# Kernel tuning notes

Measured on AMD Instinct MI355X. Metric: run time of the kernel, lower is better.

Reference implementation:

```python
import jax, jax.numpy as jnp
import numpy as np

B, T, C, HS = 4, 4096, 1024, 64


def setup_inputs() -> dict:
    key = jax.random.key(0)
    kx, kq, kk, kv = jax.random.split(key, 4)
    x = jax.random.normal(kx, (B, T, C), dtype=jnp.float32)
    s = 1.0 / np.sqrt(C)
    Wq = jax.random.normal(kq, (C, HS), dtype=jnp.float32) * s
    Wk = jax.random.normal(kk, (C, HS), dtype=jnp.float32) * s
    Wv = jax.random.normal(kv, (C, HS), dtype=jnp.float32) * s
    return {"x": x, "Wq": Wq, "Wk": Wk, "Wv": Wv}


def reference(x, Wq, Wk, Wv):
    # q,k,v: [B, T, HS]
    q = x @ Wq
    k = x @ Wk
    v = x @ Wv
    scale = k.shape[-1] ** -0.5
    # full T x T causal attention scores, as the torch module materializes
    scores = jnp.einsum('bqh,bkh->bqk', q, k) * scale  # [B, T, T]
    t = x.shape[1]
    causal = jnp.tril(jnp.ones((t, t), dtype=bool))
    scores = jnp.where(causal[None, :, :], scores, -jnp.inf)
    wei = jax.nn.softmax(scores, axis=-1)  # dropout = 0.0 (eval)
    out = jnp.einsum('bqk,bkh->bqh', wei, v)  # [B, T, HS]
    return out
```

## Files before the change

kernel.cpp:

```cpp
#include <hip/hip_runtime.h>
#include <math.h>

#define BB 4
#define TT 4096
#define CC 1024
#define HS 64
#define MM (BB*TT)

typedef __attribute__((ext_vector_type(8))) short short8;
typedef __attribute__((ext_vector_type(4))) float f32x4;
typedef __attribute__((ext_vector_type(4))) unsigned short ushort4v;

__device__ __forceinline__ unsigned short f2bf(float f) {
    union { float f; unsigned u; } v; v.f = f;
    return (unsigned short)((v.u + 0x7fffu + ((v.u >> 16) & 1u)) >> 16);
}

__global__ __launch_bounds__(256) void prep_kernel(
    const float* __restrict__ Wq, const float* __restrict__ Wk,
    const float* __restrict__ Wv, unsigned short* __restrict__ Wt)
{
    const int which = blockIdx.x >> 4;
    const int k0 = (blockIdx.x & 15) * 64;
    const float* __restrict__ W = (which == 0) ? Wq : (which == 1) ? Wk : Wv;
    const float scale = (which == 0) ? 0.125f : 1.0f;
    __shared__ unsigned short lds[64][65];
    const int t = threadIdx.x;
    #pragma unroll
    for (int i = 0; i < 16; i++) {
        int idx = t + 256 * i;
        int r = idx >> 6, n = idx & 63;
        lds[r][n] = f2bf(W[(size_t)(k0 + r) * 64 + n] * scale);
    }
    __syncthreads();
    #pragma unroll
    for (int i = 0; i < 16; i++) {
        int idx = t + 256 * i;
        int n = idx >> 6, r = idx & 63;
        Wt[(which << 16) + (n << 10) + k0 + r] = lds[r][n];
    }
}

__global__ __launch_bounds__(256, 2) void qkv_mfma(
    const float* __restrict__ x, const unsigned short* __restrict__ Wt,
    unsigned short* __restrict__ qb, unsigned short* __restrict__ kb,
    unsigned short* __restrict__ vT)
{
    const int rt = blockIdx.x;
    __shared__ unsigned short xs[32][136];
    __shared__ unsigned short ws[192][136];

    const int t = threadIdx.x;
    const int w = t >> 6;
    const int lane = t & 63;
    const int quad = lane >> 4;
    const int c = lane & 15;

    float4 xreg[4];
    short8 wreg[12];
    #pragma unroll
    for (int i = 0; i < 4; i++) {
        int idx = t + 256 * i;
        int r = idx >> 5, c4 = (idx & 31) * 4;
        xreg[i] = *(const float4*)(x + (size_t)(rt * 32 + r) * CC + c4);
    }
    #pragma unroll
    for (int i = 0; i < 12; i++) {
        int idx = t + 256 * i;
        int n = idx >> 4, c8 = (idx & 15) * 8;
        wreg[i] = *(const short8*)(Wt + (size_t)n * CC + c8);
    }

    f32x4 acc[2][3];
    #pragma unroll
    for (int mt = 0; mt < 2; mt++)
        #pragma unroll
        for (int j = 0; j < 3; j++) acc[mt][j] = (f32x4){0.f, 0.f, 0.f, 0.f};

    for (int k0 = 0; k0 < CC; k0 += 128) {
        __syncthreads();
        #pragma unroll
        for (int i = 0; i < 4; i++) {
            int idx = t + 256 * i;
            int r = idx >> 5, c4 = (idx & 31) * 4;
            ushort4v p = { f2bf(xreg[i].x), f2bf(xreg[i].y), f2bf(xreg[i].z), f2bf(xreg[i].w) };
            *(ushort4v*)&xs[r][c4] = p;
        }
        #pragma unroll
        for (int i = 0; i < 12; i++) {
            int idx = t + 256 * i;
            int n = idx >> 4, c8 = (idx & 15) * 8;
            *(short8*)&ws[n][c8] = wreg[i];
        }
        if (k0 + 128 < CC) {
            #pragma unroll
            for (int i = 0; i < 4; i++) {
                int idx = t + 256 * i;
                int r = idx >> 5, c4 = (idx & 31) * 4;
                xreg[i] = *(const float4*)(x + (size_t)(rt * 32 + r) * CC + k0 + 128 + c4);
            }
            #pragma unroll
            for (int i = 0; i < 12; i++) {
                int idx = t + 256 * i;
                int n = idx >> 4, c8 = (idx & 15) * 8;
                wreg[i] = *(const short8*)(Wt + (size_t)n * CC + k0 + 128 + c8);
            }
        }
        __syncthreads();
        #pragma unroll
        for (int ks = 0; ks < 4; ks++) {
            short8 af[2], bf[3];
            #pragma unroll
            for (int mt = 0; mt < 2; mt++)
                af[mt] = *(const short8*)&xs[16 * mt + c][ks * 32 + quad * 8];
            #pragma unroll
            for (int j = 0; j < 3; j++)
                bf[j] = *(const short8*)&ws[16 * (w + 4 * j) + c][ks * 32 + quad * 8];
            #pragma unroll
            for (int mt = 0; mt < 2; mt++)
                #pragma unroll
                for (int j = 0; j < 3; j++)
                    acc[mt][j] = __builtin_amdgcn_mfma_f32_16x16x32_bf16(af[mt], bf[j], acc[mt][j], 0, 0, 0);
        }
    }

    __syncthreads();
    unsigned short (*vtb)[72] = (unsigned short (*)[72])ws;
    #pragma unroll
    for (int mt = 0; mt < 2; mt++) {
        int grow = rt * 32 + 16 * mt + quad * 4;
        #pragma unroll
        for (int reg = 0; reg < 4; reg++) {
            qb[(size_t)(grow + reg) * HS + 16 * w + c] = f2bf(acc[mt][0][reg]);
            kb[(size_t)(grow + reg) * HS + 16 * w + c] = f2bf(acc[mt][1][reg]);
            vtb[16 * w + c][16 * mt + quad * 4 + reg] = f2bf(acc[mt][2][reg]);
        }
    }
    __syncthreads();
    {
        const int b  = rt >> 7;
        const int t0 = (rt & 127) * 32;
        int d = t >> 2, c8 = (t & 3) * 8;
        short8 v0 = *(const short8*)&vtb[d][c8];
        *(short8*)(vT + (size_t)b * HS * TT + (size_t)d * TT + t0 + c8) = v0;
    }
}

__global__ __launch_bounds__(256, 4) void attn_mfma(
    const unsigned short* __restrict__ qb, const unsigned short* __restrict__ kb,
    const unsigned short* __restrict__ vT, float* __restrict__ Opart,
    float* __restrict__ lpart)
{
    const int bid = blockIdx.x;
    const int qt = (TT / 64 - 1) - (bid >> 4);
    const int j  = (bid >> 2) & 3;
    const int b  = bid & 3;

    __shared__ unsigned short ks[64][72];
    __shared__ unsigned short vt[64][72];
    __shared__ unsigned short ps[4][16][72];

    const int t = threadIdx.x;
    const int w = t >> 6;
    const int lane = t & 63;
    const int quad = lane >> 4;
    const int c = lane & 15;
    const int qrow = qt * 64 + 16 * w;

    short8 aq[2];
    #pragma unroll
    for (int kstep = 0; kstep < 2; kstep++)
        aq[kstep] = *(const short8*)(qb + (size_t)(b * TT + qrow + c) * HS + kstep * 32 + quad * 8);

    const int nkt = (qt >= j) ? ((qt - j) >> 2) + 1 : 0;
    const unsigned short* Kb = kb + (size_t)b * TT * HS;
    const unsigned short* Vb = vT + (size_t)b * HS * TT;

    const int srow = t >> 3;
    const int sc8  = (t & 7) * 8;

    short8 kreg[2], vreg[2];
    if (nkt > 0) {
        const int kt0 = j * 64;
        #pragma unroll
        for (int i = 0; i < 2; i++) {
            kreg[i] = *(const short8*)(Kb + (size_t)(kt0 + srow + 32 * i) * HS + sc8);
            vreg[i] = *(const short8*)(Vb + (size_t)(srow + 32 * i) * TT + kt0 + sc8);
        }
    }

    float l[4] = {0.f, 0.f, 0.f, 0.f};
    f32x4 oacc[4];
    #pragma unroll
    for (int dt = 0; dt < 4; dt++) oacc[dt] = (f32x4){0.f, 0.f, 0.f, 0.f};

    for (int i = 0; i < nkt; i++) {
        const int kt = j + 4 * i;
        const int kt0 = kt * 64;
        __syncthreads();
        #pragma unroll
        for (int ii = 0; ii < 2; ii++) {
            *(short8*)&ks[srow + 32 * ii][sc8] = kreg[ii];
            *(short8*)&vt[srow + 32 * ii][sc8] = vreg[ii];
        }
        if (i + 1 < nkt) {
            const int nb = kt0 + 256;
            #pragma unroll
            for (int ii = 0; ii < 2; ii++) {
                kreg[ii] = *(const short8*)(Kb + (size_t)(nb + srow + 32 * ii) * HS + sc8);
                vreg[ii] = *(const short8*)(Vb + (size_t)(srow + 32 * ii) * TT + nb + sc8);
            }
        }
        __syncthreads();

        f32x4 sc[4];
        #pragma unroll
        for (int st = 0; st < 4; st++) sc[st] = (f32x4){0.f, 0.f, 0.f, 0.f};
        #pragma unroll
        for (int kstep = 0; kstep < 2; kstep++) {
            #pragma unroll
            for (int st = 0; st < 4; st++) {
                short8 bf = *(const short8*)&ks[16 * st + c][kstep * 32 + quad * 8];
                sc[st] = __builtin_amdgcn_mfma_f32_16x16x32_bf16(aq[kstep], bf, sc[st], 0, 0, 0);
            }
        }
        if (kt == qt) {
            #pragma unroll
            for (int st = 0; st < 4; st++)
                #pragma unroll
                for (int reg = 0; reg < 4; reg++) {
                    int kg = kt0 + 16 * st + c;
                    int qg = qrow + quad * 4 + reg;
                    float p = (kg <= qg) ? __expf(sc[st][reg]) : 0.f;
                    sc[st][reg] = p;
                    l[reg] += p;
                }
        } else {
            #pragma unroll
            for (int st = 0; st < 4; st++)
                #pragma unroll
                for (int reg = 0; reg < 4; reg++) {
                    float p = __expf(sc[st][reg]);
                    sc[st][reg] = p;
                    l[reg] += p;
                }
        }
        #pragma unroll
        for (int st = 0; st < 4; st++)
            #pragma unroll
            for (int reg = 0; reg < 4; reg++)
                ps[w][quad * 4 + reg][16 * st + c] = f2bf(sc[st][reg]);

        #pragma unroll
        for (int kstep = 0; kstep < 2; kstep++) {
            short8 ap = *(const short8*)&ps[w][c][kstep * 32 + quad * 8];
            #pragma unroll
            for (int dt = 0; dt < 4; dt++) {
                short8 bv = *(const short8*)&vt[16 * dt + c][kstep * 32 + quad * 8];
                oacc[dt] = __builtin_amdgcn_mfma_f32_16x16x32_bf16(ap, bv, oacc[dt], 0, 0, 0);
            }
        }
    }

    #pragma unroll
    for (int reg = 0; reg < 4; reg++)
        #pragma unroll
        for (int msk = 1; msk < 16; msk <<= 1)
            l[reg] += __shfl_xor(l[reg], msk);

    float* __restrict__ Oj = Opart + (size_t)j * MM * HS;
    #pragma unroll
    for (int dt = 0; dt < 4; dt++)
        #pragma unroll
        for (int reg = 0; reg < 4; reg++)
            Oj[(size_t)(b * TT + qrow + quad * 4 + reg) * HS + 16 * dt + c] = oacc[dt][reg];
    if (c == 0)
        #pragma unroll
        for (int reg = 0; reg < 4; reg++)
            lpart[(size_t)j * MM + b * TT + qrow + quad * 4 + reg] = l[reg];
}

__global__ __launch_bounds__(256) void combine_kernel(
    const float* __restrict__ Opart, const float* __restrict__ lpart,
    float* __restrict__ out)
{
    const int id = blockIdx.x * 256 + threadIdx.x;
    const int row = id >> 4;
    float l = lpart[row] + lpart[MM + row] + lpart[2 * MM + row] + lpart[3 * MM + row];
    const float4* O = (const float4*)Opart;
    const size_t stride = (size_t)MM * HS / 4;
    float4 a = O[id], b = O[id + stride], c = O[id + 2 * stride], d = O[id + 3 * stride];
    float inv = 1.f / l;
    float4 r;
    r.x = (a.x + b.x + c.x + d.x) * inv;
    r.y = (a.y + b.y + c.y + d.y) * inv;
    r.z = (a.z + b.z + c.z + d.z) * inv;
    r.w = (a.w + b.w + c.w + d.w) * inv;
    ((float4*)out)[id] = r;
}

extern "C" void kernel_launch(void* const* d_in, const int* in_sizes, int n_in,
                              void* d_out, int out_size, void* d_ws, size_t ws_size,
                              hipStream_t stream) {
    const float* x  = (const float*)d_in[0];
    const float* Wq = (const float*)d_in[1];
    const float* Wk = (const float*)d_in[2];
    const float* Wv = (const float*)d_in[3];
    float* out = (float*)d_out;

    unsigned short* Wt   = (unsigned short*)d_ws;
    unsigned short* qbuf = Wt + 3 * 64 * 1024;
    unsigned short* kbuf = qbuf + (size_t)MM * HS;
    unsigned short* vTb  = kbuf + (size_t)MM * HS;
    float* Opart = (float*)(vTb + (size_t)MM * HS);
    float* lpart = Opart + 4 * (size_t)MM * HS;

    prep_kernel<<<48, 256, 0, stream>>>(Wq, Wk, Wv, Wt);
    qkv_mfma<<<MM / 32, 256, 0, stream>>>(x, Wt, qbuf, kbuf, vTb);
    attn_mfma<<<BB * (TT / 64) * 4, 256, 0, stream>>>(qbuf, kbuf, vTb, Opart, lpart);
    combine_kernel<<<1024, 256, 0, stream>>>(Opart, lpart, out);
}
```

Before: 136.6 us.

## Retile QKV and attention kernels with register weights, transposed MFMA, larger query tiles

The QKV projection now keeps weight fragments in registers straight from global memory and works on 64-row tiles with double-buffered x in LDS. Attention handles 128 query rows per block with two 16-row subtiles per wave. It computes S^T so the probability fragments can be fed into the PV MFMA from registers, dropping the LDS round trip for P, and permutes V in LDS to match that layout. Opart is stored transposed (d-major), and the combine kernel transposes it back through LDS. These changes trade more register pressure and fewer blocks for less LDS traffic and more data reuse per block.

```diff
diff --git a/kernel.cpp b/kernel.cpp
--- a/kernel.cpp
+++ b/kernel.cpp
@@ -8,6 +8,7 @@
 #define MM (BB*TT)
 
 typedef __attribute__((ext_vector_type(8))) short short8;
+typedef __attribute__((ext_vector_type(4))) short short4v;
 typedef __attribute__((ext_vector_type(4))) float f32x4;
 typedef __attribute__((ext_vector_type(4))) unsigned short ushort4v;
 
@@ -41,14 +42,13 @@
     }
 }
 
-__global__ __launch_bounds__(256, 2) void qkv_mfma(
+__global__ __launch_bounds__(256) void qkv_mfma(
     const float* __restrict__ x, const unsigned short* __restrict__ Wt,
     unsigned short* __restrict__ qb, unsigned short* __restrict__ kb,
     unsigned short* __restrict__ vT)
 {
     const int rt = blockIdx.x;
-    __shared__ unsigned short xs[32][136];
-    __shared__ unsigned short ws[192][136];
+    __shared__ unsigned short xs[2][64][72];
 
     const int t = threadIdx.x;
     const int w = t >> 6;
@@ -56,247 +56,311 @@
     const int quad = lane >> 4;
     const int c = lane & 15;
 
+    const unsigned short* wb[3];
+    #pragma unroll
+    for (int jj = 0; jj < 3; jj++)
+        wb[jj] = Wt + (size_t)((w + 4 * jj) * 16 + c) * CC + quad * 8;
+
     float4 xreg[4];
-    short8 wreg[12];
     #pragma unroll
     for (int i = 0; i < 4; i++) {
         int idx = t + 256 * i;
-        int r = idx >> 5, c4 = (idx & 31) * 4;
-        xreg[i] = *(const float4*)(x + (size_t)(rt * 32 + r) * CC + c4);
-    }
-    #pragma unroll
-    for (int i = 0; i < 12; i++) {
-        int idx = t + 256 * i;
-        int n = idx >> 4, c8 = (idx & 15) * 8;
-        wreg[i] = *(const short8*)(Wt + (size_t)n * CC + c8);
-    }
-
-    f32x4 acc[2][3];
-    #pragma unroll
-    for (int mt = 0; mt < 2; mt++)
-        #pragma unroll
-        for (int j = 0; j < 3; j++) acc[mt][j] = (f32x4){0.f, 0.f, 0.f, 0.f};
-
-    for (int k0 = 0; k0 < CC; k0 += 128) {
-        __syncthreads();
+        xreg[i] = *(const float4*)(x + (size_t)(rt * 64 + (idx >> 4)) * CC + (idx & 15) * 4);
+    }
+    short8 wf[3][2];
+    #pragma unroll
+    for (int jj = 0; jj < 3; jj++)
+        #pragma unroll
+        for (int ks2 = 0; ks2 < 2; ks2++)
+            wf[jj][ks2] = *(const short8*)(wb[jj] + ks2 * 32);
+
+    f32x4 acc[4][3];
+    #pragma unroll
+    for (int mt = 0; mt < 4; mt++)
+        #pragma unroll
+        for (int jj = 0; jj < 3; jj++) acc[mt][jj] = (f32x4){0.f, 0.f, 0.f, 0.f};
+
+    for (int k0 = 0; k0 < CC; k0 += 64) {
+        const int p = (k0 >> 6) & 1;
         #pragma unroll
         for (int i = 0; i < 4; i++) {
             int idx = t + 256 * i;
-            int r = idx >> 5, c4 = (idx & 31) * 4;
-            ushort4v p = { f2bf(xreg[i].x), f2bf(xreg[i].y), f2bf(xreg[i].z), f2bf(xreg[i].w) };
-            *(ushort4v*)&xs[r][c4] = p;
-        }
-        #pragma unroll
-        for (int i = 0; i < 12; i++) {
-            int idx = t + 256 * i;
-            int n = idx >> 4, c8 = (idx & 15) * 8;
-            *(short8*)&ws[n][c8] = wreg[i];
-        }
-        if (k0 + 128 < CC) {
+            int r = idx >> 4, c4 = (idx & 15) * 4;
+            ushort4v pk = { f2bf(xreg[i].x), f2bf(xreg[i].y), f2bf(xreg[i].z), f2bf(xreg[i].w) };
+            *(ushort4v*)&xs[p][r][c4] = pk;
+        }
+        if (k0 + 64 < CC) {
             #pragma unroll
             for (int i = 0; i < 4; i++) {
                 int idx = t + 256 * i;
-                int r = idx >> 5, c4 = (idx & 31) * 4;
-                xreg[i] = *(const float4*)(x + (size_t)(rt * 32 + r) * CC + k0 + 128 + c4);
-            }
-            #pragma unroll
-            for (int i = 0; i < 12; i++) {
-                int idx = t + 256 * i;
-                int n = idx >> 4, c8 = (idx & 15) * 8;
-                wreg[i] = *(const short8*)(Wt + (size_t)n * CC + k0 + 128 + c8);
+                xreg[i] = *(const float4*)(x + (size_t)(rt * 64 + (idx >> 4)) * CC + k0 + 64 + (idx & 15) * 4);
             }
         }
         __syncthreads();
-        #pragma unroll
-        for (int ks = 0; ks < 4; ks++) {
-            short8 af[2], bf[3];
-            #pragma unroll
-            for (int mt = 0; mt < 2; mt++)
-                af[mt] = *(const short8*)&xs[16 * mt + c][ks * 32 + quad * 8];
-            #pragma unroll
-            for (int j = 0; j < 3; j++)
-                bf[j] = *(const short8*)&ws[16 * (w + 4 * j) + c][ks * 32 + quad * 8];
-            #pragma unroll
-            for (int mt = 0; mt < 2; mt++)
-                #pragma unroll
-                for (int j = 0; j < 3; j++)
-                    acc[mt][j] = __builtin_amdgcn_mfma_f32_16x16x32_bf16(af[mt], bf[j], acc[mt][j], 0, 0, 0);
+        short8 wn[3][2];
+        if (k0 + 64 < CC) {
+            #pragma unroll
+            for (int jj = 0; jj < 3; jj++)
+                #pragma unroll
+                for (int ks2 = 0; ks2 < 2; ks2++)
+                    wn[jj][ks2] = *(const short8*)(wb[jj] + k0 + 64 + ks2 * 32);
+        }
+        #pragma unroll
+        for (int ks2 = 0; ks2 < 2; ks2++) {
+            short8 af[4];
+            #pragma unroll
+            for (int mt = 0; mt < 4; mt++)
+                af[mt] = *(const short8*)&xs[p][16 * mt + c][ks2 * 32 + quad * 8];
+            #pragma unroll
+            for (int mt = 0; mt < 4; mt++)
+                #pragma unroll
+                for (int jj = 0; jj < 3; jj++)
+                    acc[mt][jj] = __builtin_amdgcn_mfma_f32_16x16x32_bf16(af[mt], wf[jj][ks2], acc[mt][jj], 0, 0, 0);
+        }
+        if (k0 + 64 < CC) {
+            #pragma unroll
+            for (int jj = 0; jj < 3; jj++)
+                #pragma unroll
+                for (int ks2 = 0; ks2 < 2; ks2++)
+                    wf[jj][ks2] = wn[jj][ks2];
         }
     }
 
     __syncthreads();
-    unsigned short (*vtb)[72] = (unsigned short (*)[72])ws;
-    #pragma unroll
-    for (int mt = 0; mt < 2; mt++) {
-        int grow = rt * 32 + 16 * mt + quad * 4;
+    unsigned short (*vtb)[72] = xs[0];
+    #pragma unroll
+    for (int mt = 0; mt < 4; mt++) {
         #pragma unroll
         for (int reg = 0; reg < 4; reg++) {
-            qb[(size_t)(grow + reg) * HS + 16 * w + c] = f2bf(acc[mt][0][reg]);
-            kb[(size_t)(grow + reg) * HS + 16 * w + c] = f2bf(acc[mt][1][reg]);
-            vtb[16 * w + c][16 * mt + quad * 4 + reg] = f2bf(acc[mt][2][reg]);
+            int lrow = 16 * mt + quad * 4 + reg;
+            size_t grow = (size_t)(rt * 64 + lrow);
+            qb[grow * HS + 16 * w + c] = f2bf(acc[mt][0][reg]);
+            kb[grow * HS + 16 * w + c] = f2bf(acc[mt][1][reg]);
+            vtb[16 * w + c][lrow] = f2bf(acc[mt][2][reg]);
         }
     }
     __syncthreads();
     {
-        const int b  = rt >> 7;
-        const int t0 = (rt & 127) * 32;
-        int d = t >> 2, c8 = (t & 3) * 8;
-        short8 v0 = *(const short8*)&vtb[d][c8];
-        *(short8*)(vT + (size_t)b * HS * TT + (size_t)d * TT + t0 + c8) = v0;
-    }
-}
-
-__global__ __launch_bounds__(256, 4) void attn_mfma(
+        const int b  = rt >> 6;
+        const int t0 = (rt & 63) * 64;
+        #pragma unroll
+        for (int i = 0; i < 2; i++) {
+            int idx = t + 256 * i;
+            int d = idx >> 3, c8 = (idx & 7) * 8;
+            *(short8*)(vT + ((size_t)b * HS + d) * TT + t0 + c8) = *(const short8*)&vtb[d][c8];
+        }
+    }
+}
+
+__global__ __launch_bounds__(256, 2) void attn_mfma(
     const unsigned short* __restrict__ qb, const unsigned short* __restrict__ kb,
     const unsigned short* __restrict__ vT, float* __restrict__ Opart,
     float* __restrict__ lpart)
 {
     const int bid = blockIdx.x;
-    const int qt = (TT / 64 - 1) - (bid >> 4);
+    const int qt = (TT / 128 - 1) - (bid >> 4);
     const int j  = (bid >> 2) & 3;
     const int b  = bid & 3;
 
     __shared__ unsigned short ks[64][72];
     __shared__ unsigned short vt[64][72];
-    __shared__ unsigned short ps[4][16][72];
 
     const int t = threadIdx.x;
     const int w = t >> 6;
     const int lane = t & 63;
     const int quad = lane >> 4;
     const int c = lane & 15;
-    const int qrow = qt * 64 + 16 * w;
-
-    short8 aq[2];
-    #pragma unroll
-    for (int kstep = 0; kstep < 2; kstep++)
-        aq[kstep] = *(const short8*)(qb + (size_t)(b * TT + qrow + c) * HS + kstep * 32 + quad * 8);
-
-    const int nkt = (qt >= j) ? ((qt - j) >> 2) + 1 : 0;
+    const int qrow = qt * 128 + 32 * w;
+
+    short8 aq[2][2];
+    #pragma unroll
+    for (int qt2 = 0; qt2 < 2; qt2++)
+        #pragma unroll
+        for (int ksd = 0; ksd < 2; ksd++)
+            aq[qt2][ksd] = *(const short8*)(qb + (size_t)(b * TT + qrow + 16 * qt2 + c) * HS + ksd * 32 + quad * 8);
+
+    const int lastkt = 2 * qt + 1;
+    const int nkt = (lastkt >= j) ? ((lastkt - j) >> 2) + 1 : 0;
     const unsigned short* Kb = kb + (size_t)b * TT * HS;
     const unsigned short* Vb = vT + (size_t)b * HS * TT;
-
-    const int srow = t >> 3;
-    const int sc8  = (t & 7) * 8;
 
     short8 kreg[2], vreg[2];
     if (nkt > 0) {
         const int kt0 = j * 64;
         #pragma unroll
         for (int i = 0; i < 2; i++) {
-            kreg[i] = *(const short8*)(Kb + (size_t)(kt0 + srow + 32 * i) * HS + sc8);
-            vreg[i] = *(const short8*)(Vb + (size_t)(srow + 32 * i) * TT + kt0 + sc8);
-        }
-    }
-
-    float l[4] = {0.f, 0.f, 0.f, 0.f};
-    f32x4 oacc[4];
-    #pragma unroll
-    for (int dt = 0; dt < 4; dt++) oacc[dt] = (f32x4){0.f, 0.f, 0.f, 0.f};
-
-    for (int i = 0; i < nkt; i++) {
-        const int kt = j + 4 * i;
-        const int kt0 = kt * 64;
+            int idx = t + 256 * i;
+            int row = idx >> 3, c8 = (idx & 7) * 8;
+            kreg[i] = *(const short8*)(Kb + (size_t)(kt0 + row) * HS + c8);
+            vreg[i] = *(const short8*)(Vb + (size_t)row * TT + kt0 + c8);
+        }
+    }
+
+    float lsum[2] = {0.f, 0.f};
+    f32x4 oacc[2][4];
+    #pragma unroll
+    for (int qt2 = 0; qt2 < 2; qt2++)
+        #pragma unroll
+        for (int dt = 0; dt < 4; dt++) oacc[qt2][dt] = (f32x4){0.f, 0.f, 0.f, 0.f};
+
+    for (int it = 0; it < nkt; it++) {
+        const int kt0 = (j + 4 * it) * 64;
         __syncthreads();
         #pragma unroll
-        for (int ii = 0; ii < 2; ii++) {
-            *(short8*)&ks[srow + 32 * ii][sc8] = kreg[ii];
-            *(short8*)&vt[srow + 32 * ii][sc8] = vreg[ii];
-        }
-        if (i + 1 < nkt) {
+        for (int i = 0; i < 2; i++) {
+            int idx = t + 256 * i;
+            int row = idx >> 3, c8 = (idx & 7) * 8;
+            *(short8*)&ks[row][c8] = kreg[i];
+            int t32 = c8 & 32, r32 = c8 & 31;
+            int p0 = t32 + ((r32 & 8) << 1) + ((r32 >> 4) << 2);
+            short8 v = vreg[i];
+            short4v lo = { v[0], v[1], v[2], v[3] };
+            short4v hi = { v[4], v[5], v[6], v[7] };
+            *(short4v*)&vt[row][p0]     = lo;
+            *(short4v*)&vt[row][p0 + 8] = hi;
+        }
+        if (it + 1 < nkt) {
             const int nb = kt0 + 256;
             #pragma unroll
-            for (int ii = 0; ii < 2; ii++) {
-                kreg[ii] = *(const short8*)(Kb + (size_t)(nb + srow + 32 * ii) * HS + sc8);
-                vreg[ii] = *(const short8*)(Vb + (size_t)(srow + 32 * ii) * TT + nb + sc8);
+            for (int i = 0; i < 2; i++) {
+                int idx = t + 256 * i;
+                int row = idx >> 3, c8 = (idx & 7) * 8;
+                kreg[i] = *(const short8*)(Kb + (size_t)(nb + row) * HS + c8);
+                vreg[i] = *(const short8*)(Vb + (size_t)row * TT + nb + c8);
             }
         }
         __syncthreads();
 
-        f32x4 sc[4];
-        #pragma unroll
-        for (int st = 0; st < 4; st++) sc[st] = (f32x4){0.f, 0.f, 0.f, 0.f};
-        #pragma unroll
-        for (int kstep = 0; kstep < 2; kstep++) {
-            #pragma unroll
-            for (int st = 0; st < 4; st++) {
-                short8 bf = *(const short8*)&ks[16 * st + c][kstep * 32 + quad * 8];
-                sc[st] = __builtin_amdgcn_mfma_f32_16x16x32_bf16(aq[kstep], bf, sc[st], 0, 0, 0);
-            }
-        }
-        if (kt == qt) {
+        if (kt0 <= qrow + 31) {
+            f32x4 sc[4][2];
             #pragma unroll
             for (int st = 0; st < 4; st++)
                 #pragma unroll
-                for (int reg = 0; reg < 4; reg++) {
-                    int kg = kt0 + 16 * st + c;
-                    int qg = qrow + quad * 4 + reg;
-                    float p = (kg <= qg) ? __expf(sc[st][reg]) : 0.f;
-                    sc[st][reg] = p;
-                    l[reg] += p;
+                for (int qt2 = 0; qt2 < 2; qt2++) sc[st][qt2] = (f32x4){0.f, 0.f, 0.f, 0.f};
+            #pragma unroll
+            for (int ksd = 0; ksd < 2; ksd++) {
+                short8 kf[4];
+                #pragma unroll
+                for (int st = 0; st < 4; st++)
+                    kf[st] = *(const short8*)&ks[16 * st + c][ksd * 32 + quad * 8];
+                #pragma unroll
+                for (int st = 0; st < 4; st++)
+                    #pragma unroll
+                    for (int qt2 = 0; qt2 < 2; qt2++)
+                        sc[st][qt2] = __builtin_amdgcn_mfma_f32_16x16x32_bf16(kf[st], aq[qt2][ksd], sc[st][qt2], 0, 0, 0);
+            }
+            const bool needmask = (kt0 + 63 > qrow);
+            #pragma unroll
+            for (int st = 0; st < 4; st++)
+                #pragma unroll
+                for (int qt2 = 0; qt2 < 2; qt2++)
+                    #pragma unroll
+                    for (int reg = 0; reg < 4; reg++) {
+                        float p;
+                        if (needmask) {
+                            int key = kt0 + 16 * st + quad * 4 + reg;
+                            int qg  = qrow + 16 * qt2 + c;
+                            p = (key <= qg) ? __expf(sc[st][qt2][reg]) : 0.f;
+                        } else {
+                            p = __expf(sc[st][qt2][reg]);
+                        }
+                        sc[st][qt2][reg] = p;
+                        lsum[qt2] += p;
+                    }
+            short8 pf[2][2];
+            #pragma unroll
+            for (int qt2 = 0; qt2 < 2; qt2++)
+                #pragma unroll
+                for (int t32 = 0; t32 < 2; t32++) {
+                    short8 pk;
+                    #pragma unroll
+                    for (int reg = 0; reg < 4; reg++) {
+                        pk[reg]     = (short)f2bf(sc[2 * t32][qt2][reg]);
+                        pk[reg + 4] = (short)f2bf(sc[2 * t32 + 1][qt2][reg]);
+                    }
+                    pf[qt2][t32] = pk;
                 }
-        } else {
-            #pragma unroll
-            for (int st = 0; st < 4; st++)
-                #pragma unroll
-                for (int reg = 0; reg < 4; reg++) {
-                    float p = __expf(sc[st][reg]);
-                    sc[st][reg] = p;
-                    l[reg] += p;
-                }
-        }
-        #pragma unroll
-        for (int st = 0; st < 4; st++)
-            #pragma unroll
-            for (int reg = 0; reg < 4; reg++)
-                ps[w][quad * 4 + reg][16 * st + c] = f2bf(sc[st][reg]);
-
-        #pragma unroll
-        for (int kstep = 0; kstep < 2; kstep++) {
-            short8 ap = *(const short8*)&ps[w][c][kstep * 32 + quad * 8];
-            #pragma unroll
-            for (int dt = 0; dt < 4; dt++) {
-                short8 bv = *(const short8*)&vt[16 * dt + c][kstep * 32 + quad * 8];
-                oacc[dt] = __builtin_amdgcn_mfma_f32_16x16x32_bf16(ap, bv, oacc[dt], 0, 0, 0);
-            }
-        }
-    }
-
-    #pragma unroll
-    for (int reg = 0; reg < 4; reg++)
-        #pragma unroll
-        for (int msk = 1; msk < 16; msk <<= 1)
-            l[reg] += __shfl_xor(l[reg], msk);
-
-    float* __restrict__ Oj = Opart + (size_t)j * MM * HS;
-    #pragma unroll
-    for (int dt = 0; dt < 4; dt++)
-        #pragma unroll
-        for (int reg = 0; reg < 4; reg++)
-            Oj[(size_t)(b * TT + qrow + quad * 4 + reg) * HS + 16 * dt + c] = oacc[dt][reg];
-    if (c == 0)
-        #pragma unroll
-        for (int reg = 0; reg < 4; reg++)
-            lpart[(size_t)j * MM + b * TT + qrow + quad * 4 + reg] = l[reg];
+            #pragma unroll
+            for (int t32 = 0; t32 < 2; t32++) {
+                short8 vf[4];
+                #pragma unroll
+                for (int dt = 0; dt < 4; dt++)
+                    vf[dt] = *(const short8*)&vt[16 * dt + c][t32 * 32 + quad * 8];
+                #pragma unroll
+                for (int dt = 0; dt < 4; dt++)
+                    #pragma unroll
+                    for (int qt2 = 0; qt2 < 2; qt2++)
+                        oacc[qt2][dt] = __builtin_amdgcn_mfma_f32_16x16x32_bf16(vf[dt], pf[qt2][t32], oacc[qt2][dt], 0, 0, 0);
+            }
+        }
+    }
+
+    #pragma unroll
+    for (int qt2 = 0; qt2 < 2; qt2++) {
+        lsum[qt2] += __shfl_xor(lsum[qt2], 16);
+        lsum[qt2] += __shfl_xor(lsum[qt2], 32);
+    }
+    float* __restrict__ Oj = Opart + (size_t)(j * 4 + b) * HS * TT;
+    #pragma unroll
+    for (int qt2 = 0; qt2 < 2; qt2++)
+        #pragma unroll
+        for (int dt = 0; dt < 4; dt++)
+            #pragma unroll
+            for (int reg = 0; reg < 4; reg++) {
+                int d = 16 * dt + quad * 4 + reg;
+                Oj[(size_t)d * TT + qrow + 16 * qt2 + c] = oacc[qt2][dt][reg];
+            }
+    if (lane < 16)
+        #pragma unroll
+        for (int qt2 = 0; qt2 < 2; qt2++)
+            lpart[(size_t)(j * 4 + b) * TT + qrow + 16 * qt2 + lane] = lsum[qt2];
 }
 
 __global__ __launch_bounds__(256) void combine_kernel(
     const float* __restrict__ Opart, const float* __restrict__ lpart,
     float* __restrict__ out)
 {
-    const int id = blockIdx.x * 256 + threadIdx.x;
-    const int row = id >> 4;
-    float l = lpart[row] + lpart[MM + row] + lpart[2 * MM + row] + lpart[3 * MM + row];
-    const float4* O = (const float4*)Opart;
-    const size_t stride = (size_t)MM * HS / 4;
-    float4 a = O[id], b = O[id + stride], c = O[id + 2 * stride], d = O[id + 3 * stride];
-    float inv = 1.f / l;
-    float4 r;
-    r.x = (a.x + b.x + c.x + d.x) * inv;
-    r.y = (a.y + b.y + c.y + d.y) * inv;
-    r.z = (a.z + b.z + c.z + d.z) * inv;
-    r.w = (a.w + b.w + c.w + d.w) * inv;
-    ((float4*)out)[id] = r;
+    const int b  = blockIdx.x & 3;
+    const int q0 = (blockIdx.x >> 2) * 64;
+    __shared__ float ts[64][68];
+    const int t = threadIdx.x;
+
+    float4 s[4] = {};
+    #pragma unroll
+    for (int jj = 0; jj < 4; jj++) {
+        const float* Oj = Opart + (size_t)(jj * 4 + b) * HS * TT;
+        #pragma unroll
+        for (int i = 0; i < 4; i++) {
+            int idx = t + 256 * i;
+            int d = idx >> 4, c4 = (idx & 15) * 4;
+            float4 v = *(const float4*)(Oj + (size_t)d * TT + q0 + c4);
+            s[i].x += v.x; s[i].y += v.y; s[i].z += v.z; s[i].w += v.w;
+        }
+    }
+    #pragma unroll
+    for (int i = 0; i < 4; i++) {
+        int idx = t + 256 * i;
+        int d = idx >> 4, c4 = (idx & 15) * 4;
+        *(float4*)&ts[d][c4] = s[i];
+    }
+    __syncthreads();
+
+    const int q  = t >> 2;
+    const int dc = (t & 3) * 16;
+    float l = 0.f;
+    #pragma unroll
+    for (int jj = 0; jj < 4; jj++)
+        l += lpart[(size_t)(jj * 4 + b) * TT + q0 + q];
+    const float inv = 1.f / l;
+    #pragma unroll
+    for (int g = 0; g < 4; g++) {
+        float4 r;
+        r.x = ts[dc + g * 4 + 0][q] * inv;
+        r.y = ts[dc + g * 4 + 1][q] * inv;
+        r.z = ts[dc + g * 4 + 2][q] * inv;
+        r.w = ts[dc + g * 4 + 3][q] * inv;
+        *(float4*)(out + (size_t)(b * TT + q0 + q) * HS + dc + g * 4) = r;
+    }
 }
 
 extern "C" void kernel_launch(void* const* d_in, const int* in_sizes, int n_in,
@@ -316,7 +380,7 @@
     float* lpart = Opart + 4 * (size_t)MM * HS;
 
     prep_kernel<<<48, 256, 0, stream>>>(Wq, Wk, Wv, Wt);
-    qkv_mfma<<<MM / 32, 256, 0, stream>>>(x, Wt, qbuf, kbuf, vTb);
-    attn_mfma<<<BB * (TT / 64) * 4, 256, 0, stream>>>(qbuf, kbuf, vTb, Opart, lpart);
-    combine_kernel<<<1024, 256, 0, stream>>>(Opart, lpart, out);
-}
+    qkv_mfma<<<MM / 64, 256, 0, stream>>>(x, Wt, qbuf, kbuf, vTb);
+    attn_mfma<<<BB * (TT / 128) * 4, 256, 0, stream>>>(qbuf, kbuf, vTb, Opart, lpart);
+    combine_kernel<<<BB * (TT / 64), 256, 0, stream>>>(Opart, lpart, out);
+}
```

New measurement: 151.9 us. 11.1% more time.
